# Optimization experiments

Hardware: AMD Instinct MI355X
Metric: run time of the kernel (lower is better)

The kernel has to match this reference:

```python
import jax, jax.numpy as jnp
import numpy as np

B, S, D, H = 4, 4096, 1024, 1024


def log_g(x):
    # where(x >= 0, log(relu(x) + 0.5), -softplus(-x)); relu(x)+0.5 >= 0.5 so log is safe
    return jnp.where(x >= 0, jnp.log(jax.nn.relu(x) + 0.5), -jax.nn.softplus(-x))


def setup_inputs() -> dict:
    key = jax.random.key(0)
    ks = jax.random.split(key, 8)
    scale = 1.0 / np.sqrt(D)
    return {
        "x_t": jax.random.normal(ks[0], (B, S, D), dtype=jnp.float32),
        "pre_h": jax.random.normal(ks[1], (B, 1, H), dtype=jnp.float32),
        "W_f": jax.random.uniform(ks[2], (H, D), jnp.float32, -scale, scale),
        "b_f": jax.random.uniform(ks[3], (H,), jnp.float32, -scale, scale),
        "W_i": jax.random.uniform(ks[4], (H, D), jnp.float32, -scale, scale),
        "b_i": jax.random.uniform(ks[5], (H,), jnp.float32, -scale, scale),
        "W_h": jax.random.uniform(ks[6], (H, D), jnp.float32, -scale, scale),
        "b_h": jax.random.uniform(ks[7], (H,), jnp.float32, -scale, scale),
    }


def reference(x_t, pre_h, W_f, b_f, W_i, b_i, W_h, b_h):
    sp = jax.nn.softplus
    f_pre = jnp.einsum("bsd,hd->bsh", x_t, W_f) + b_f
    i_pre = jnp.einsum("bsd,hd->bsh", x_t, W_i) + b_i
    h_pre = jnp.einsum("bsd,hd->bsh", x_t, W_h) + b_h

    diff = sp(-f_pre) - sp(-i_pre)
    log_f = -sp(diff)        # (B, S, H)
    log_i = -sp(-diff)       # (B, S, H)

    log_h0 = log_g(pre_h)                 # (B, 1, H)
    log_tilde_h = log_g(h_pre)            # (B, S, H)
    log_values = jnp.concatenate([log_h0, log_i + log_tilde_h], axis=1)  # (B, S+1, H)

    # parallel_scan_log: pad cumsum at END of seq dim (as in source: F.pad(..., (0,0,0,1)))
    a_star = jnp.pad(jnp.cumsum(log_f, axis=1), ((0, 0), (0, 1), (0, 0)))  # (B, S+1, H)
    log_h0_plus_b_star = jax.lax.cumlogsumexp(log_values - a_star, axis=1)
    log_h = a_star + log_h0_plus_b_star
    return jnp.exp(log_h)[:, 1:]  # (B, S, H)
```

## Files before the change

kernel.cpp:

```cpp
#include <hip/hip_runtime.h>
#include <hip/hip_bf16.h>
#include <math.h>

#define B_DIM 4
#define S_DIM 4096
#define K_DIM 1024
#define H_DIM 1024
#define M_DIM (B_DIM * S_DIM)

#define BMT 256
#define BNT 128
#define KT_ITERS (K_DIM / 32)

#define NCHUNK 256
#define CLEN (S_DIM / NCHUNK)

typedef __attribute__((ext_vector_type(8))) _Float16 f16x8;
typedef __attribute__((ext_vector_type(4))) _Float16 f16x4;
typedef __attribute__((ext_vector_type(4))) float f32x4;

__device__ __forceinline__ float sp_f(float x) {
    return fmaxf(x, 0.0f) + __logf(1.0f + __expf(-fabsf(x)));
}
__device__ __forceinline__ float log_g_f(float x) {
    return (x >= 0.0f) ? __logf(x + 0.5f) : -sp_f(-x);
}
__device__ __forceinline__ float logaddexp_f(float a, float b) {
    float m = fmaxf(a, b);
    return m + __logf(1.0f + __expf(-fabsf(a - b)));
}
__device__ __forceinline__ float exp_sat(float x) {
    return __expf(fminf(x, 85.0f));
}

__device__ __forceinline__ void gl_lds16(const void* g, void* l) {
    __builtin_amdgcn_global_load_lds(
        (const __attribute__((address_space(1))) unsigned int*)g,
        (__attribute__((address_space(3))) unsigned int*)l, 16, 0, 0);
}

#define NX_F4 (M_DIM * K_DIM / 4)
#define NW_F4 (H_DIM * K_DIM / 4)
__global__ __launch_bounds__(256) void conv_all(
    const float* __restrict__ x, const float* __restrict__ Wf,
    const float* __restrict__ Wi, const float* __restrict__ Wh,
    _Float16* __restrict__ xh, _Float16* __restrict__ wh)
{
    int i = blockIdx.x * 256 + threadIdx.x;
    const float* src;
    _Float16* dst;
    int j;
    if (i < NX_F4) {
        src = x; dst = xh; j = i;
    } else {
        int t = i - NX_F4;
        int g = t >> 18;
        j = t & (NW_F4 - 1);
        src = (g == 0) ? Wf : (g == 1) ? Wi : Wh;
        dst = wh + (size_t)g * H_DIM * K_DIM;
    }
    float4 v = ((const float4*)src)[j];
    f16x4 o = {(_Float16)v.x, (_Float16)v.y, (_Float16)v.z, (_Float16)v.w};
    ((f16x4*)dst)[j] = o;
}

__global__ __launch_bounds__(512, 2) void gemm3(
    const _Float16* __restrict__ xh,
    const _Float16* __restrict__ wh,
    const float* __restrict__ bfp, const float* __restrict__ bip,
    const float* __restrict__ bhp,
    _Float16* __restrict__ lf_out, _Float16* __restrict__ w_out)
{
    __shared__ __align__(16) char smem0[40960];
    __shared__ __align__(16) char smem1[40960];
    __shared__ __align__(16) char smem2[40960];

    const int tid = threadIdx.x;
    const int lane = tid & 63;
    const int wv = tid >> 6;
    const int wm = wv >> 2;
    const int wn = wv & 3;

    const int row0 = blockIdx.y * BMT;
    const int col0 = blockIdx.x * BNT;

    const int sswz = (tid & 3) ^ ((tid >> 3) & 3);
    unsigned ga0 = (unsigned)(((row0 + (tid >> 2)) * K_DIM + sswz * 8) * 2);
    unsigned ga1 = ga0 + 128 * K_DIM * 2;
    unsigned gb0 = (unsigned)(((0 * H_DIM + col0 + (tid >> 2)) * K_DIM + sswz * 8) * 2);
    unsigned gb1 = (unsigned)(((1 * H_DIM + col0 + (tid >> 2)) * K_DIM + sswz * 8) * 2);
    unsigned gb2 = (unsigned)(((2 * H_DIM + col0 + (tid >> 2)) * K_DIM + sswz * 8) * 2);

    const char* __restrict__ px = (const char*)xh;
    const char* __restrict__ pw = (const char*)wh;

    const int ar = wm * 128 + (lane & 15);
    const int aoff0 = ar * 64 + ((((lane >> 4) ^ ((ar >> 1) & 3))) << 4);
    const int bc = wn * 32 + (lane & 15);
    const int boff0 = 16384 + bc * 64 + ((((lane >> 4) ^ ((bc >> 1) & 3))) << 4);

    f32x4 acc[3][8][2];
#pragma unroll
    for (int g = 0; g < 3; ++g)
#pragma unroll
        for (int mi = 0; mi < 8; ++mi)
#pragma unroll
            for (int nj = 0; nj < 2; ++nj)
                acc[g][mi][nj] = (f32x4){0.f, 0.f, 0.f, 0.f};

#define STAGE5(S) do { \
    gl_lds16(px + ga0, (S) + tid * 16); \
    gl_lds16(px + ga1, (S) + 8192 + tid * 16); \
    gl_lds16(pw + gb0, (S) + 16384 + tid * 16); \
    gl_lds16(pw + gb1, (S) + 24576 + tid * 16); \
    gl_lds16(pw + gb2, (S) + 32768 + tid * 16); \
    ga0 += 64; ga1 += 64; gb0 += 64; gb1 += 64; gb2 += 64; } while (0)

#define SBAR do { \
    __builtin_amdgcn_sched_barrier(0); \
    __builtin_amdgcn_s_barrier(); } while (0)

#define LGKM0 do { \
    asm volatile("s_waitcnt lgkmcnt(0)" ::: "memory"); \
    __builtin_amdgcn_sched_barrier(0); } while (0)

#define MFMA12(A0, A1, MI0, MI1) do { \
    __builtin_amdgcn_s_setprio(1); \
    _Pragma("unroll") \
    for (int g = 0; g < 3; ++g) { \
        acc[g][MI0][0] = __builtin_amdgcn_mfma_f32_16x16x32_f16(A0, b_[g][0], acc[g][MI0][0], 0, 0, 0); \
        acc[g][MI0][1] = __builtin_amdgcn_mfma_f32_16x16x32_f16(A0, b_[g][1], acc[g][MI0][1], 0, 0, 0); \
        acc[g][MI1][0] = __builtin_amdgcn_mfma_f32_16x16x32_f16(A1, b_[g][0], acc[g][MI1][0], 0, 0, 0); \
        acc[g][MI1][1] = __builtin_amdgcn_mfma_f32_16x16x32_f16(A1, b_[g][1], acc[g][MI1][1], 0, 0, 0); \
    } \
    __builtin_amdgcn_s_setprio(0); } while (0)

#define TILE(CUR, STG, DOSTAGE, VN) do { \
    f16x8 b_[3][2]; \
    _Pragma("unroll") \
    for (int g = 0; g < 3; ++g) { \
        b_[g][0] = *(const f16x8*)((CUR) + g * 8192 + boff0); \
        b_[g][1] = *(const f16x8*)((CUR) + g * 8192 + boff0 + 1024); \
    } \
    f16x8 a0_ = *(const f16x8*)((CUR) + aoff0); \
    f16x8 a1_ = *(const f16x8*)((CUR) + aoff0 + 1024); \
    if (DOSTAGE) { \
        gl_lds16(px + ga0, (STG) + tid * 16); \
        gl_lds16(px + ga1, (STG) + 8192 + tid * 16); \
    } \
    SBAR; LGKM0; \
    MFMA12(a0_, a1_, 0, 1); \
    f16x8 a2_ = *(const f16x8*)((CUR) + aoff0 + 2048); \
    f16x8 a3_ = *(const f16x8*)((CUR) + aoff0 + 3072); \
    if (DOSTAGE) gl_lds16(pw + gb0, (STG) + 16384 + tid * 16); \
    SBAR; LGKM0; \
    MFMA12(a2_, a3_, 2, 3); \
    f16x8 a4_ = *(const f16x8*)((CUR) + aoff0 + 4096); \
    f16x8 a5_ = *(const f16x8*)((CUR) + aoff0 + 5120); \
    if (DOSTAGE) gl_lds16(pw + gb1, (STG) + 24576 + tid * 16); \
    SBAR; LGKM0; \
    MFMA12(a4_, a5_, 4, 5); \
    f16x8 a6_ = *(const f16x8*)((CUR) + aoff0 + 6144); \
    f16x8 a7_ = *(const f16x8*)((CUR) + aoff0 + 7168); \
    if (DOSTAGE) { \
        gl_lds16(pw + gb2, (STG) + 32768 + tid * 16); \
        ga0 += 64; ga1 += 64; gb0 += 64; gb1 += 64; gb2 += 64; \
    } \
    SBAR; LGKM0; \
    MFMA12(a6_, a7_, 6, 7); \
    asm volatile("s_waitcnt vmcnt(" #VN ")" ::: "memory"); \
    SBAR; } while (0)

    STAGE5(smem0);
    STAGE5(smem1);
    asm volatile("s_waitcnt vmcnt(5)" ::: "memory");
    SBAR;

#pragma unroll 1
    for (int it = 0; it < 10; ++it) {
        TILE(smem0, smem2, 1, 5);
        TILE(smem1, smem0, 1, 5);
        TILE(smem2, smem1, 1, 5);
    }
    TILE(smem0, smem2, 0, 0);
    TILE(smem1, smem0, 0, 0);

#undef TILE
#undef MFMA12
#undef LGKM0
#undef SBAR
#undef STAGE5

    int nidx[2];
    float bfv[2], biv[2], bhv[2];
#pragma unroll
    for (int nj = 0; nj < 2; ++nj) {
        nidx[nj] = col0 + wn * 32 + nj * 16 + (lane & 15);
        bfv[nj] = bfp[nidx[nj]];
        biv[nj] = bip[nidx[nj]];
        bhv[nj] = bhp[nidx[nj]];
    }
#pragma unroll
    for (int mi = 0; mi < 8; ++mi) {
#pragma unroll
        for (int r = 0; r < 4; ++r) {
            int m = row0 + wm * 128 + mi * 16 + ((lane >> 4) << 2) + r;
#pragma unroll
            for (int nj = 0; nj < 2; ++nj) {
                float f_pre = acc[0][mi][nj][r] + bfv[nj];
                float i_pre = acc[1][mi][nj][r] + biv[nj];
                float h_pre = acc[2][mi][nj][r] + bhv[nj];
                float diff = sp_f(-f_pre) - sp_f(-i_pre);
                float lfv = -sp_f(diff);
                float wv_ = -sp_f(-diff) + log_g_f(h_pre);
                size_t o = (size_t)m * H_DIM + nidx[nj];
                lf_out[o] = (_Float16)lfv;
                w_out[o] = (_Float16)wv_;
            }
        }
    }
}

__global__ __launch_bounds__(256) void scan_pass_a(
    const _Float16* __restrict__ lf, const _Float16* __restrict__ w,
    float2* __restrict__ agg)
{
    int tid = blockIdx.x * blockDim.x + threadIdx.x;
    int hq = tid & (H_DIM / 4 - 1);
    int b = (tid >> 8) & (B_DIM - 1);
    int q = tid >> 10;
    int h0 = hq * 4;

    int tstart = q * CLEN + 1;
    int tend = (q == NCHUNK - 1) ? (S_DIM - 1) : (q * CLEN + CLEN);

    size_t idx = (size_t)(b * S_DIM + tstart) * H_DIM + h0;
    float c[4] = {0.f, 0.f, 0.f, 0.f};
    float r[4] = {-INFINITY, -INFINITY, -INFINITY, -INFINITY};
#pragma unroll 4
    for (int t = tstart; t <= tend; ++t) {
        f16x4 lv = *(const f16x4*)(lf + idx);
        f16x4 wv = *(const f16x4*)(w + idx - H_DIM);
#pragma unroll
        for (int j = 0; j < 4; ++j) {
            c[j] += (float)lv[j];
            r[j] = logaddexp_f(r[j], (float)wv[j] - c[j]);
        }
        idx += H_DIM;
    }
#pragma unroll
    for (int j = 0; j < 4; ++j)
        agg[(size_t)(b * H_DIM + h0 + j) * NCHUNK + q] = make_float2(c[j], r[j]);
}

__global__ __launch_bounds__(256) void scan_pass_b(
    const _Float16* __restrict__ lf, const float* __restrict__ preh,
    float2* aggp)
{
    int lane = threadIdx.x & 63;
    int col = blockIdx.x * 4 + (threadIdx.x >> 6);
    int h = col & (H_DIM - 1);
    int b = col >> 10;

    size_t base = (size_t)col * NCHUNK + lane * 4;
    float2 a0 = aggp[base + 0];
    float2 a1 = aggp[base + 1];
    float2 a2 = aggp[base + 2];
    float2 a3 = aggp[base + 3];

    float sc = a0.x, sr = a0.y;
    sr = logaddexp_f(sr, a1.y - sc); sc += a1.x;
    sr = logaddexp_f(sr, a2.y - sc); sc += a2.x;
    sr = logaddexp_f(sr, a3.y - sc); sc += a3.x;

    float c = sc, r = sr;
#pragma unroll
    for (int off = 1; off < 64; off <<= 1) {
        float pc = __shfl_up(c, off, 64);
        float pr = __shfl_up(r, off, 64);
        if (lane >= off) {
            r = logaddexp_f(pr, r - pc);
            c = pc + c;
        }
    }
    float ec = __shfl_up(c, 1, 64);
    float er = __shfl_up(r, 1, 64);
    if (lane == 0) { ec = 0.0f; er = -INFINITY; }

    float pc0 = ec, pr0 = er;
    float pc1 = pc0, pr1 = logaddexp_f(pr0, a0.y - pc0); pc1 += a0.x;
    float pc2 = pc1, pr2 = logaddexp_f(pr1, a1.y - pc1); pc2 += a1.x;
    float pc3 = pc2, pr3 = logaddexp_f(pr2, a2.y - pc2); pc3 += a2.x;

    float lf0 = (float)lf[(size_t)(b * S_DIM) * H_DIM + h];
    float C0 = lf0;
    float R0 = log_g_f(preh[b * H_DIM + h]) - lf0;
    aggp[base + 0] = make_float2(C0 + pc0, logaddexp_f(R0, pr0 - C0));
    aggp[base + 1] = make_float2(C0 + pc1, logaddexp_f(R0, pr1 - C0));
    aggp[base + 2] = make_float2(C0 + pc2, logaddexp_f(R0, pr2 - C0));
    aggp[base + 3] = make_float2(C0 + pc3, logaddexp_f(R0, pr3 - C0));
}

__global__ __launch_bounds__(256) void scan_pass_c(
    const _Float16* __restrict__ lf, const _Float16* __restrict__ w,
    const float2* __restrict__ prefix, float* __restrict__ out)
{
    int tid = blockIdx.x * blockDim.x + threadIdx.x;
    int hq = tid & (H_DIM / 4 - 1);
    int b = (tid >> 8) & (B_DIM - 1);
    int q = tid >> 10;
    int h0 = hq * 4;

    float C[4], R[4];
#pragma unroll
    for (int j = 0; j < 4; ++j) {
        float2 p = prefix[(size_t)(b * H_DIM + h0 + j) * NCHUNK + q];
        C[j] = p.x; R[j] = p.y;
    }

    int tstart = q * CLEN + 1;
    int tend = (q == NCHUNK - 1) ? (S_DIM - 1) : (q * CLEN + CLEN);

    size_t idx = (size_t)(b * S_DIM + tstart) * H_DIM + h0;
#pragma unroll 4
    for (int t = tstart; t <= tend; ++t) {
        f16x4 lv = *(const f16x4*)(lf + idx);
        f16x4 wv = *(const f16x4*)(w + idx - H_DIM);
        float4 ov;
        C[0] += (float)lv[0]; R[0] = logaddexp_f(R[0], (float)wv[0] - C[0]); ov.x = exp_sat(C[0] + R[0]);
        C[1] += (float)lv[1]; R[1] = logaddexp_f(R[1], (float)wv[1] - C[1]); ov.y = exp_sat(C[1] + R[1]);
        C[2] += (float)lv[2]; R[2] = logaddexp_f(R[2], (float)wv[2] - C[2]); ov.z = exp_sat(C[2] + R[2]);
        C[3] += (float)lv[3]; R[3] = logaddexp_f(R[3], (float)wv[3] - C[3]); ov.w = exp_sat(C[3] + R[3]);
        *(float4*)(out + idx - H_DIM) = ov;
        idx += H_DIM;
    }
    if (q == NCHUNK - 1) {
        f16x4 wv = *(const f16x4*)(w + idx - H_DIM);
        float4 ov;
        ov.x = exp_sat(logaddexp_f(R[0], (float)wv[0]));
        ov.y = exp_sat(logaddexp_f(R[1], (float)wv[1]));
        ov.z = exp_sat(logaddexp_f(R[2], (float)wv[2]));
        ov.w = exp_sat(logaddexp_f(R[3], (float)wv[3]));
        *(float4*)(out + idx - H_DIM) = ov;
    }
}

extern "C" void kernel_launch(void* const* d_in, const int* in_sizes, int n_in,
                              void* d_out, int out_size, void* d_ws, size_t ws_size,
                              hipStream_t stream) {
    const float* x    = (const float*)d_in[0];
    const float* preh = (const float*)d_in[1];
    const float* Wf   = (const float*)d_in[2];
    const float* bf   = (const float*)d_in[3];
    const float* Wi   = (const float*)d_in[4];
    const float* bi   = (const float*)d_in[5];
    const float* Wh   = (const float*)d_in[6];
    const float* bh   = (const float*)d_in[7];
    float* out = (float*)d_out;

    _Float16* xh = (_Float16*)d_ws;
    _Float16* wh = xh + (size_t)M_DIM * K_DIM;
    _Float16* lf = wh + (size_t)3 * H_DIM * K_DIM;
    _Float16* wbuf = lf + (size_t)M_DIM * H_DIM;
    float2* agg = (float2*)xh;

    conv_all<<<(NX_F4 + 3 * NW_F4) / 256, 256, 0, stream>>>(x, Wf, Wi, Wh, xh, wh);

    gemm3<<<dim3(H_DIM / BNT, M_DIM / BMT), 512, 0, stream>>>(
        xh, wh, bf, bi, bh, lf, wbuf);

    scan_pass_a<<<(B_DIM * H_DIM * NCHUNK / 4) / 256, 256, 0, stream>>>(lf, wbuf, agg);
    scan_pass_b<<<(B_DIM * H_DIM) / 4, 256, 0, stream>>>(lf, preh, agg);
    scan_pass_c<<<(B_DIM * H_DIM * NCHUNK / 4) / 256, 256, 0, stream>>>(lf, wbuf, agg, out);
}
```

Before: 319.9 us.

## Fuse three scan passes into one cooperative kernel with grid syncs

Merges the chunk-reduce, chunk-prefix and chunk-apply scan kernels into a single cooperative kernel launched with 1024 blocks, separated by grid.sync() barriers. This removes two kernel launches and their inter-kernel gaps. In exchange it depends on all 1024 blocks being co-resident (launch bound of 4 blocks per CU) and pays for two grid-wide barriers. The launch return value is not checked, so a failed cooperative launch would go unnoticed.

```diff
diff --git a/kernel.cpp b/kernel.cpp
--- a/kernel.cpp
+++ b/kernel.cpp
@@ -1,6 +1,9 @@
 #include <hip/hip_runtime.h>
 #include <hip/hip_bf16.h>
+#include <hip/hip_cooperative_groups.h>
 #include <math.h>
+
+namespace cg = cooperative_groups;
 
 #define B_DIM 4
 #define S_DIM 4096
@@ -221,127 +224,128 @@
     }
 }
 
-__global__ __launch_bounds__(256) void scan_pass_a(
+__global__ __launch_bounds__(256, 4) void fused_scan(
     const _Float16* __restrict__ lf, const _Float16* __restrict__ w,
-    float2* __restrict__ agg)
+    const float* __restrict__ preh, float2* agg, float* __restrict__ out)
 {
-    int tid = blockIdx.x * blockDim.x + threadIdx.x;
-    int hq = tid & (H_DIM / 4 - 1);
-    int b = (tid >> 8) & (B_DIM - 1);
-    int q = tid >> 10;
-    int h0 = hq * 4;
-
-    int tstart = q * CLEN + 1;
-    int tend = (q == NCHUNK - 1) ? (S_DIM - 1) : (q * CLEN + CLEN);
-
-    size_t idx = (size_t)(b * S_DIM + tstart) * H_DIM + h0;
-    float c[4] = {0.f, 0.f, 0.f, 0.f};
-    float r[4] = {-INFINITY, -INFINITY, -INFINITY, -INFINITY};
+    cg::grid_group grid = cg::this_grid();
+    const int tid = blockIdx.x * 256 + threadIdx.x;
+
+    {
+        int hq = tid & (H_DIM / 4 - 1);
+        int b = (tid >> 8) & (B_DIM - 1);
+        int q = tid >> 10;
+        int h0 = hq * 4;
+
+        int tstart = q * CLEN + 1;
+        int tend = (q == NCHUNK - 1) ? (S_DIM - 1) : (q * CLEN + CLEN);
+
+        size_t idx = (size_t)(b * S_DIM + tstart) * H_DIM + h0;
+        float c[4] = {0.f, 0.f, 0.f, 0.f};
+        float r[4] = {-INFINITY, -INFINITY, -INFINITY, -INFINITY};
 #pragma unroll 4
-    for (int t = tstart; t <= tend; ++t) {
-        f16x4 lv = *(const f16x4*)(lf + idx);
-        f16x4 wv = *(const f16x4*)(w + idx - H_DIM);
+        for (int t = tstart; t <= tend; ++t) {
+            f16x4 lv = *(const f16x4*)(lf + idx);
+            f16x4 wv = *(const f16x4*)(w + idx - H_DIM);
+#pragma unroll
+            for (int j = 0; j < 4; ++j) {
+                c[j] += (float)lv[j];
+                r[j] = logaddexp_f(r[j], (float)wv[j] - c[j]);
+            }
+            idx += H_DIM;
+        }
+#pragma unroll
+        for (int j = 0; j < 4; ++j)
+            agg[(size_t)(b * H_DIM + h0 + j) * NCHUNK + q] = make_float2(c[j], r[j]);
+    }
+
+    grid.sync();
+
+    {
+        int lane = threadIdx.x & 63;
+        int col = blockIdx.x * 4 + (threadIdx.x >> 6);
+        int h = col & (H_DIM - 1);
+        int b = col >> 10;
+
+        size_t base = (size_t)col * NCHUNK + lane * 4;
+        float2 a0 = agg[base + 0];
+        float2 a1 = agg[base + 1];
+        float2 a2 = agg[base + 2];
+        float2 a3 = agg[base + 3];
+
+        float sc = a0.x, sr = a0.y;
+        sr = logaddexp_f(sr, a1.y - sc); sc += a1.x;
+        sr = logaddexp_f(sr, a2.y - sc); sc += a2.x;
+        sr = logaddexp_f(sr, a3.y - sc); sc += a3.x;
+
+        float c = sc, r = sr;
+#pragma unroll
+        for (int off = 1; off < 64; off <<= 1) {
+            float pc = __shfl_up(c, off, 64);
+            float pr = __shfl_up(r, off, 64);
+            if (lane >= off) {
+                r = logaddexp_f(pr, r - pc);
+                c = pc + c;
+            }
+        }
+        float ec = __shfl_up(c, 1, 64);
+        float er = __shfl_up(r, 1, 64);
+        if (lane == 0) { ec = 0.0f; er = -INFINITY; }
+
+        float pc0 = ec, pr0 = er;
+        float pc1 = pc0, pr1 = logaddexp_f(pr0, a0.y - pc0); pc1 += a0.x;
+        float pc2 = pc1, pr2 = logaddexp_f(pr1, a1.y - pc1); pc2 += a1.x;
+        float pc3 = pc2, pr3 = logaddexp_f(pr2, a2.y - pc2); pc3 += a2.x;
+
+        float lf0 = (float)lf[(size_t)(b * S_DIM) * H_DIM + h];
+        float C0 = lf0;
+        float R0 = log_g_f(preh[b * H_DIM + h]) - lf0;
+        agg[base + 0] = make_float2(C0 + pc0, logaddexp_f(R0, pr0 - C0));
+        agg[base + 1] = make_float2(C0 + pc1, logaddexp_f(R0, pr1 - C0));
+        agg[base + 2] = make_float2(C0 + pc2, logaddexp_f(R0, pr2 - C0));
+        agg[base + 3] = make_float2(C0 + pc3, logaddexp_f(R0, pr3 - C0));
+    }
+
+    grid.sync();
+
+    {
+        int hq = tid & (H_DIM / 4 - 1);
+        int b = (tid >> 8) & (B_DIM - 1);
+        int q = tid >> 10;
+        int h0 = hq * 4;
+
+        float C[4], R[4];
 #pragma unroll
         for (int j = 0; j < 4; ++j) {
-            c[j] += (float)lv[j];
-            r[j] = logaddexp_f(r[j], (float)wv[j] - c[j]);
-        }
-        idx += H_DIM;
-    }
-#pragma unroll
-    for (int j = 0; j < 4; ++j)
-        agg[(size_t)(b * H_DIM + h0 + j) * NCHUNK + q] = make_float2(c[j], r[j]);
-}
-
-__global__ __launch_bounds__(256) void scan_pass_b(
-    const _Float16* __restrict__ lf, const float* __restrict__ preh,
-    float2* aggp)
-{
-    int lane = threadIdx.x & 63;
-    int col = blockIdx.x * 4 + (threadIdx.x >> 6);
-    int h = col & (H_DIM - 1);
-    int b = col >> 10;
-
-    size_t base = (size_t)col * NCHUNK + lane * 4;
-    float2 a0 = aggp[base + 0];
-    float2 a1 = aggp[base + 1];
-    float2 a2 = aggp[base + 2];
-    float2 a3 = aggp[base + 3];
-
-    float sc = a0.x, sr = a0.y;
-    sr = logaddexp_f(sr, a1.y - sc); sc += a1.x;
-    sr = logaddexp_f(sr, a2.y - sc); sc += a2.x;
-    sr = logaddexp_f(sr, a3.y - sc); sc += a3.x;
-
-    float c = sc, r = sr;
-#pragma unroll
-    for (int off = 1; off < 64; off <<= 1) {
-        float pc = __shfl_up(c, off, 64);
-        float pr = __shfl_up(r, off, 64);
-        if (lane >= off) {
-            r = logaddexp_f(pr, r - pc);
-            c = pc + c;
-        }
-    }
-    float ec = __shfl_up(c, 1, 64);
-    float er = __shfl_up(r, 1, 64);
-    if (lane == 0) { ec = 0.0f; er = -INFINITY; }
-
-    float pc0 = ec, pr0 = er;
-    float pc1 = pc0, pr1 = logaddexp_f(pr0, a0.y - pc0); pc1 += a0.x;
-    float pc2 = pc1, pr2 = logaddexp_f(pr1, a1.y - pc1); pc2 += a1.x;
-    float pc3 = pc2, pr3 = logaddexp_f(pr2, a2.y - pc2); pc3 += a2.x;
-
-    float lf0 = (float)lf[(size_t)(b * S_DIM) * H_DIM + h];
-    float C0 = lf0;
-    float R0 = log_g_f(preh[b * H_DIM + h]) - lf0;
-    aggp[base + 0] = make_float2(C0 + pc0, logaddexp_f(R0, pr0 - C0));
-    aggp[base + 1] = make_float2(C0 + pc1, logaddexp_f(R0, pr1 - C0));
-    aggp[base + 2] = make_float2(C0 + pc2, logaddexp_f(R0, pr2 - C0));
-    aggp[base + 3] = make_float2(C0 + pc3, logaddexp_f(R0, pr3 - C0));
-}
-
-__global__ __launch_bounds__(256) void scan_pass_c(
-    const _Float16* __restrict__ lf, const _Float16* __restrict__ w,
-    const float2* __restrict__ prefix, float* __restrict__ out)
-{
-    int tid = blockIdx.x * blockDim.x + threadIdx.x;
-    int hq = tid & (H_DIM / 4 - 1);
-    int b = (tid >> 8) & (B_DIM - 1);
-    int q = tid >> 10;
-    int h0 = hq * 4;
-
-    float C[4], R[4];
-#pragma unroll
-    for (int j = 0; j < 4; ++j) {
-        float2 p = prefix[(size_t)(b * H_DIM + h0 + j) * NCHUNK + q];
-        C[j] = p.x; R[j] = p.y;
-    }
-
-    int tstart = q * CLEN + 1;
-    int tend = (q == NCHUNK - 1) ? (S_DIM - 1) : (q * CLEN + CLEN);
-
-    size_t idx = (size_t)(b * S_DIM + tstart) * H_DIM + h0;
+            float2 p = agg[(size_t)(b * H_DIM + h0 + j) * NCHUNK + q];
+            C[j] = p.x; R[j] = p.y;
+        }
+
+        int tstart = q * CLEN + 1;
+        int tend = (q == NCHUNK - 1) ? (S_DIM - 1) : (q * CLEN + CLEN);
+
+        size_t idx = (size_t)(b * S_DIM + tstart) * H_DIM + h0;
 #pragma unroll 4
-    for (int t = tstart; t <= tend; ++t) {
-        f16x4 lv = *(const f16x4*)(lf + idx);
-        f16x4 wv = *(const f16x4*)(w + idx - H_DIM);
-        float4 ov;
-        C[0] += (float)lv[0]; R[0] = logaddexp_f(R[0], (float)wv[0] - C[0]); ov.x = exp_sat(C[0] + R[0]);
-        C[1] += (float)lv[1]; R[1] = logaddexp_f(R[1], (float)wv[1] - C[1]); ov.y = exp_sat(C[1] + R[1]);
-        C[2] += (float)lv[2]; R[2] = logaddexp_f(R[2], (float)wv[2] - C[2]); ov.z = exp_sat(C[2] + R[2]);
-        C[3] += (float)lv[3]; R[3] = logaddexp_f(R[3], (float)wv[3] - C[3]); ov.w = exp_sat(C[3] + R[3]);
-        *(float4*)(out + idx - H_DIM) = ov;
-        idx += H_DIM;
-    }
-    if (q == NCHUNK - 1) {
-        f16x4 wv = *(const f16x4*)(w + idx - H_DIM);
-        float4 ov;
-        ov.x = exp_sat(logaddexp_f(R[0], (float)wv[0]));
-        ov.y = exp_sat(logaddexp_f(R[1], (float)wv[1]));
-        ov.z = exp_sat(logaddexp_f(R[2], (float)wv[2]));
-        ov.w = exp_sat(logaddexp_f(R[3], (float)wv[3]));
-        *(float4*)(out + idx - H_DIM) = ov;
+        for (int t = tstart; t <= tend; ++t) {
+            f16x4 lv = *(const f16x4*)(lf + idx);
+            f16x4 wv = *(const f16x4*)(w + idx - H_DIM);
+            float4 ov;
+            C[0] += (float)lv[0]; R[0] = logaddexp_f(R[0], (float)wv[0] - C[0]); ov.x = exp_sat(C[0] + R[0]);
+            C[1] += (float)lv[1]; R[1] = logaddexp_f(R[1], (float)wv[1] - C[1]); ov.y = exp_sat(C[1] + R[1]);
+            C[2] += (float)lv[2]; R[2] = logaddexp_f(R[2], (float)wv[2] - C[2]); ov.z = exp_sat(C[2] + R[2]);
+            C[3] += (float)lv[3]; R[3] = logaddexp_f(R[3], (float)wv[3] - C[3]); ov.w = exp_sat(C[3] + R[3]);
+            *(float4*)(out + idx - H_DIM) = ov;
+            idx += H_DIM;
+        }
+        if (q == NCHUNK - 1) {
+            f16x4 wv = *(const f16x4*)(w + idx - H_DIM);
+            float4 ov;
+            ov.x = exp_sat(logaddexp_f(R[0], (float)wv[0]));
+            ov.y = exp_sat(logaddexp_f(R[1], (float)wv[1]));
+            ov.z = exp_sat(logaddexp_f(R[2], (float)wv[2]));
+            ov.w = exp_sat(logaddexp_f(R[3], (float)wv[3]));
+            *(float4*)(out + idx - H_DIM) = ov;
+        }
     }
 }
 
@@ -369,7 +373,11 @@
     gemm3<<<dim3(H_DIM / BNT, M_DIM / BMT), 512, 0, stream>>>(
         xh, wh, bf, bi, bh, lf, wbuf);
 
-    scan_pass_a<<<(B_DIM * H_DIM * NCHUNK / 4) / 256, 256, 0, stream>>>(lf, wbuf, agg);
-    scan_pass_b<<<(B_DIM * H_DIM) / 4, 256, 0, stream>>>(lf, preh, agg);
-    scan_pass_c<<<(B_DIM * H_DIM * NCHUNK / 4) / 256, 256, 0, stream>>>(lf, wbuf, agg, out);
-}
+    const _Float16* lf_c = lf;
+    const _Float16* w_c = wbuf;
+    void* args[] = {(void*)&lf_c, (void*)&w_c, (void*)&preh,
+                    (void*)&agg, (void*)&out};
+    hipLaunchCooperativeKernel((const void*)fused_scan,
+                               dim3(B_DIM * H_DIM / 4), dim3(256),
+                               args, 0, stream);
+}
```

After: 590.7 us. +84.6%, slower.
